# Performance work log

Measured on AMD Instinct MI355X. Metric: run time of the kernel, lower is better.

## Reference

```python
import jax, jax.numpy as jnp
import numpy as np

B, S, D, H = 4, 2048, 1024, 16
DK = D // H


def setup_inputs() -> dict:
    key = jax.random.key(0)
    ks = jax.random.split(key, 12)
    s = 1.0 / np.sqrt(D)
    inp = {
        "q": jax.random.normal(ks[0], (B, S, D), jnp.float32),
        "k": jax.random.normal(ks[1], (B, S, D), jnp.float32),
        "v": jax.random.normal(ks[2], (B, S, D), jnp.float32),
        # causal mask, broadcastable over batch and heads
        "mask": jnp.tril(jnp.ones((S, S), jnp.int32))[None, None, :, :],
        "Wq": jax.random.uniform(ks[3], (D, D), jnp.float32, -s, s),
        "bq": jax.random.uniform(ks[4], (D,), jnp.float32, -s, s),
        "Wk": jax.random.uniform(ks[5], (D, D), jnp.float32, -s, s),
        "bk": jax.random.uniform(ks[6], (D,), jnp.float32, -s, s),
        "Wv": jax.random.uniform(ks[7], (D, D), jnp.float32, -s, s),
        "bv": jax.random.uniform(ks[8], (D,), jnp.float32, -s, s),
        "Wo": jax.random.uniform(ks[9], (D, D), jnp.float32, -s, s),
        "bo": jax.random.uniform(ks[10], (D,), jnp.float32, -s, s),
    }
    return inp


def reference(q, k, v, mask, Wq, bq, Wk, bk, Wv, bv, Wo, bo):
    def split_heads(x):  # [B,S,D] -> [B,H,S,DK]
        return x.reshape(B, S, H, DK).transpose(0, 2, 1, 3)

    qh = split_heads(q @ Wq.T + bq)
    kh = split_heads(k @ Wk.T + bk)
    vh = split_heads(v @ Wv.T + bv)

    scores = jnp.einsum("bhqd,bhkd->bhqk", qh, kh) / jnp.sqrt(jnp.float32(DK))
    scores = jnp.where(mask == 0, jnp.float32(-1e9), scores)
    attn = jax.nn.softmax(scores, axis=-1)
    out = jnp.einsum("bhqk,bhkd->bhqd", attn, vh)
    out = out.transpose(0, 2, 1, 3).reshape(B, S, D)
    return out @ Wo.T + bo
```

## Files before the change

### kernel.cpp

```cpp
#include <hip/hip_runtime.h>
#include <cstdint>

#define Bb 4
#define Ss 2048
#define Dd 1024
#define Hh 16

typedef unsigned short u16;
typedef unsigned int u32;
typedef __attribute__((ext_vector_type(8))) short short8;
typedef __attribute__((ext_vector_type(8))) _Float16 half8;
typedef __attribute__((ext_vector_type(2))) __fp16 fp16x2;
typedef __attribute__((ext_vector_type(4))) float floatx4;
typedef __attribute__((address_space(3))) u32 lds_u32;
typedef const __attribute__((address_space(1))) u32 glob_u32;

__device__ __forceinline__ u16 f2bf(float x) {
  union { float f; u32 u; } v; v.f = x;
  u32 r = v.u + 0x7fffu + ((v.u >> 16) & 1u);
  return (u16)(r >> 16);
}

__global__ __launch_bounds__(256) void cvt_many(const float* __restrict__ s0,
                                                const float* __restrict__ s1,
                                                const float* __restrict__ s2,
                                                const float* __restrict__ s3,
                                                u16* __restrict__ d0,
                                                u16* __restrict__ d1,
                                                u16* __restrict__ d2,
                                                u16* __restrict__ d3, int n8) {
  int z = blockIdx.y;
  const float* s = z == 0 ? s0 : z == 1 ? s1 : z == 2 ? s2 : s3;
  u16* d = z == 0 ? d0 : z == 1 ? d1 : z == 2 ? d2 : d3;
  int i = blockIdx.x * 256 + threadIdx.x;
  if (i >= n8) return;
  const float4* sp = (const float4*)s;
  float4 a = sp[2 * i], b = sp[2 * i + 1];
  u32 w0 = (u32)f2bf(a.x) | ((u32)f2bf(a.y) << 16);
  u32 w1 = (u32)f2bf(a.z) | ((u32)f2bf(a.w) << 16);
  u32 w2 = (u32)f2bf(b.x) | ((u32)f2bf(b.y) << 16);
  u32 w3 = (u32)f2bf(b.z) | ((u32)f2bf(b.w) << 16);
  ((uint4*)d)[i] = make_uint4(w0, w1, w2, w3);
}

template <int MODE>
__device__ __forceinline__ void gemm_body(const u16* __restrict__ A,
                                          const u16* __restrict__ Bw,
                                          const float* __restrict__ bias,
                                          void* __restrict__ Cout, float scale) {
  __shared__ u16 As[128 * 64];
  __shared__ u16 Bs[128 * 64];
  int tid = threadIdx.x;
  int wave = tid >> 6, lane = tid & 63;
  int quad = lane >> 4, l16 = lane & 15;
  int m0 = blockIdx.x * 128, n0 = blockIdx.y * 128;
  int wr = (wave >> 1) * 64, wc = (wave & 1) * 64;
  int s7 = l16 & 7;
  int srow = wave * 8 + (lane >> 3);
  int gcol = (((lane & 7) ^ (lane >> 3)) << 3);

  floatx4 vzero = {0.f, 0.f, 0.f, 0.f};
  floatx4 acc[4][4];
#pragma unroll
  for (int i = 0; i < 4; ++i)
#pragma unroll
    for (int j = 0; j < 4; ++j) acc[i][j] = vzero;

  for (int kt = 0; kt < Dd; kt += 64) {
    __syncthreads();
#pragma unroll
    for (int c = 0; c < 4; ++c) {
      int r = c * 32 + srow;
      __builtin_amdgcn_global_load_lds(
          (glob_u32*)&A[(size_t)(m0 + r) * Dd + kt + gcol],
          (lds_u32*)&As[(c * 32 + wave * 8) * 64], 16, 0, 0);
      __builtin_amdgcn_global_load_lds(
          (glob_u32*)&Bw[(size_t)(n0 + r) * Dd + kt + gcol],
          (lds_u32*)&Bs[(c * 32 + wave * 8) * 64], 16, 0, 0);
    }
    __syncthreads();
#pragma unroll
    for (int kk = 0; kk < 2; ++kk) {
      short8 af[4], bf[4];
#pragma unroll
      for (int i = 0; i < 4; ++i)
        af[i] = *(const short8*)&As[(wr + i * 16 + l16) * 64 + (((quad + 4 * kk) ^ s7) << 3)];
#pragma unroll
      for (int j = 0; j < 4; ++j)
        bf[j] = *(const short8*)&Bs[(wc + j * 16 + l16) * 64 + (((quad + 4 * kk) ^ s7) << 3)];
#pragma unroll
      for (int i = 0; i < 4; ++i)
#pragma unroll
        for (int j = 0; j < 4; ++j)
          acc[i][j] = __builtin_amdgcn_mfma_f32_16x16x32_bf16(af[i], bf[j], acc[i][j], 0, 0, 0);
    }
  }

#pragma unroll
  for (int i = 0; i < 4; ++i) {
#pragma unroll
    for (int j = 0; j < 4; ++j) {
#pragma unroll
      for (int r = 0; r < 4; ++r) {
        int m = m0 + wr + i * 16 + quad * 4 + r;
        int n = n0 + wc + j * 16 + l16;
        float val = (acc[i][j][r] + bias[n]) * scale;
        if (MODE == 0) {
          int b = m >> 11, s = m & (Ss - 1);
          int h = n >> 6, dk = n & 63;
          ((u16*)Cout)[((((size_t)b * Hh + h) * Ss + s) << 6) + dk] = f2bf(val);
        } else {
          ((float*)Cout)[(size_t)m * Dd + n] = val;
        }
      }
    }
  }
}

__global__ __launch_bounds__(256) void gemm_qkv(const u16* qb, const u16* kb, const u16* vb,
                                                const u16* Wq, const u16* Wk, const u16* Wv,
                                                const float* bq, const float* bk, const float* bv,
                                                u16* qo, u16* ko, u16* vo) {
  const float K1 = 0.18033688f;
  int z = blockIdx.z;
  const u16* A = z == 0 ? qb : z == 1 ? kb : vb;
  const u16* W = z == 0 ? Wq : z == 1 ? Wk : Wv;
  const float* bi = z == 0 ? bq : z == 1 ? bk : bv;
  u16* o = z == 0 ? qo : z == 1 ? ko : vo;
  gemm_body<0>(A, W, bi, o, z == 0 ? K1 : 1.0f);
}

__global__ __launch_bounds__(256) void gemm_out(const u16* A, const u16* W,
                                                const float* bi, float* o) {
  gemm_body<1>(A, W, bi, o, 1.0f);
}

__global__ __launch_bounds__(256) void transpose_v(const u16* __restrict__ in,
                                                   _Float16* __restrict__ out) {
  __shared__ u16 T[64 * 72];
  int bh = blockIdx.y, s0 = blockIdx.x * 64, tid = threadIdx.x;
#pragma unroll
  for (int c = 0; c < 2; ++c) {
    int e = c * 2048 + tid * 8;
    int r = e >> 6, col = e & 63;
    *(uint4*)&T[r * 72 + col] = *(const uint4*)&in[((size_t)bh * Ss + s0 + r) * 64 + col];
  }
  __syncthreads();
#pragma unroll
  for (int c = 0; c < 2; ++c) {
    int e = c * 2048 + tid * 8;
    int d = e >> 6, sc = e & 63;
    _Float16 tmp[8];
#pragma unroll
    for (int j = 0; j < 8; ++j) {
      union { u32 u; float f; } cv;
      cv.u = (u32)T[(sc + j) * 72 + d] << 16;
      tmp[j] = (_Float16)cv.f;
    }
    *(uint4*)&out[((size_t)bh * 64 + d) * Ss + s0 + sc] = *(uint4*)tmp;
  }
}

#define MFIX 4.0f
__global__ __launch_bounds__(256) void attn_kernel(const u16* __restrict__ qh,
                                                   const u16* __restrict__ kh,
                                                   const _Float16* __restrict__ vT,
                                                   u16* __restrict__ ctx) {
  __shared__ u16 Kt[64 * 64];
  __shared__ _Float16 Vt[64 * 64];
  __shared__ _Float16 Ps[4][16 * 64];

  int tid = threadIdx.x, w = tid >> 6, lane = tid & 63;
  int quad = lane >> 4, l16 = lane & 15;
  int s7 = l16 & 7, s2 = (l16 & 7) << 1;
  int bh = blockIdx.x;
  int sp = blockIdx.y;
  const u16* Q = qh + (size_t)bh * Ss * 64;
  const u16* K = kh + (size_t)bh * Ss * 64;
  const _Float16* V = vT + (size_t)bh * 64 * Ss;

  int R[2] = {64 * sp + 16 * w, 64 * (31 - sp) + 16 * w};
  short8 qf[2][2];
#pragma unroll
  for (int qm = 0; qm < 2; ++qm)
#pragma unroll
    for (int kk = 0; kk < 2; ++kk)
      qf[qm][kk] = *(const short8*)&Q[(size_t)(R[qm] + l16) * 64 + kk * 32 + quad * 8];

  floatx4 vzero = {0.f, 0.f, 0.f, 0.f};
  floatx4 o[2][4];
#pragma unroll
  for (int qm = 0; qm < 2; ++qm)
#pragma unroll
    for (int nt = 0; nt < 4; ++nt) o[qm][nt] = vzero;
  float l_i[2] = {0.f, 0.f};

  int srow = tid >> 3, kc = tid & 7;
  int nkt = 32 - sp;
  for (int kt = 0; kt < nkt; ++kt) {
    int k0 = kt * 64;
    __syncthreads();
#pragma unroll
    for (int c = 0; c < 2; ++c) {
      int r = c * 32 + srow;
      int wcol = ((kc ^ (r & 7)) << 3);
      *(uint4*)&Kt[r * 64 + wcol] = *(const uint4*)&K[(size_t)(k0 + r) * 64 + kc * 8];
      *(uint4*)&Vt[r * 64 + wcol] = *(const uint4*)&V[(size_t)r * Ss + k0 + kc * 8];
    }
    __syncthreads();

    half8 vf[4][2];
#pragma unroll
    for (int nt = 0; nt < 4; ++nt)
#pragma unroll
      for (int kk = 0; kk < 2; ++kk)
        vf[nt][kk] = *(const half8*)&Vt[(nt * 16 + l16) * 64 + (((quad + 4 * kk) ^ s7) << 3)];

#pragma unroll
    for (int qm = 0; qm < 2; ++qm) {
      int Rq = R[qm];
      if (k0 > Rq + 15) continue;
      floatx4 sc[4];
#pragma unroll
      for (int t4 = 0; t4 < 4; ++t4) {
        short8 kf0 = *(const short8*)&Kt[(t4 * 16 + l16) * 64 + ((quad ^ s7) << 3)];
        short8 kf1 = *(const short8*)&Kt[(t4 * 16 + l16) * 64 + (((quad + 4) ^ s7) << 3)];
        floatx4 s = __builtin_amdgcn_mfma_f32_16x16x32_bf16(kf0, qf[qm][0], vzero, 0, 0, 0);
        sc[t4] = __builtin_amdgcn_mfma_f32_16x16x32_bf16(kf1, qf[qm][1], s, 0, 0, 0);
      }
      int qrow = Rq + l16;
      if (k0 + 63 > Rq) {
#pragma unroll
        for (int t4 = 0; t4 < 4; ++t4)
#pragma unroll
          for (int r = 0; r < 4; ++r) {
            int key = k0 + t4 * 16 + quad * 4 + r;
            if (key > qrow) sc[t4][r] = -3e38f;
          }
      }
      float rs = 0.f;
      _Float16* Pw = &Ps[w][0];
#pragma unroll
      for (int t4 = 0; t4 < 4; ++t4) {
        float p0 = __builtin_amdgcn_exp2f(sc[t4][0] - MFIX);
        float p1 = __builtin_amdgcn_exp2f(sc[t4][1] - MFIX);
        float p2 = __builtin_amdgcn_exp2f(sc[t4][2] - MFIX);
        float p3 = __builtin_amdgcn_exp2f(sc[t4][3] - MFIX);
        rs += (p0 + p1) + (p2 + p3);
        union { fp16x2 h[2]; uint2 u; } cv;
        cv.h[0] = __builtin_amdgcn_cvt_pkrtz(p0, p1);
        cv.h[1] = __builtin_amdgcn_cvt_pkrtz(p2, p3);
        *(uint2*)&Pw[l16 * 64 + (((4 * t4 + quad) ^ s2) << 2)] = cv.u;
      }
      rs += __shfl_xor(rs, 16, 64);
      rs += __shfl_xor(rs, 32, 64);
      l_i[qm] += rs;
#pragma unroll
      for (int kk = 0; kk < 2; ++kk) {
        half8 pf = *(const half8*)&Pw[l16 * 64 + (((8 * kk + 2 * quad) ^ s2) << 2)];
#pragma unroll
        for (int nt = 0; nt < 4; ++nt)
          o[qm][nt] = __builtin_amdgcn_mfma_f32_16x16x32_f16(pf, vf[nt][kk], o[qm][nt], 0, 0, 0);
      }
    }
  }

  int b = bh >> 4, h = bh & 15;
#pragma unroll
  for (int qm = 0; qm < 2; ++qm) {
    float lr[4];
#pragma unroll
    for (int r = 0; r < 4; ++r) lr[r] = __shfl(l_i[qm], quad * 4 + r, 64);
#pragma unroll
    for (int nt = 0; nt < 4; ++nt)
#pragma unroll
      for (int r = 0; r < 4; ++r) {
        int s = R[qm] + quad * 4 + r;
        int dk = nt * 16 + l16;
        ctx[((size_t)b * Ss + s) * Dd + h * 64 + dk] = f2bf(o[qm][nt][r] / lr[r]);
      }
  }
}

extern "C" void kernel_launch(void* const* d_in, const int* in_sizes, int n_in,
                              void* d_out, int out_size, void* d_ws, size_t ws_size,
                              hipStream_t stream) {
  const float* q = (const float*)d_in[0];
  const float* k = (const float*)d_in[1];
  const float* v = (const float*)d_in[2];
  const float* Wq = (const float*)d_in[4];
  const float* bq = (const float*)d_in[5];
  const float* Wk = (const float*)d_in[6];
  const float* bk = (const float*)d_in[7];
  const float* Wv = (const float*)d_in[8];
  const float* bv = (const float*)d_in[9];
  const float* Wo = (const float*)d_in[10];
  const float* bo = (const float*)d_in[11];

  char* ws = (char*)d_ws;
  const size_t MB = 1024 * 1024;
  u16* qb = (u16*)(ws + 0 * MB);
  u16* kb = (u16*)(ws + 16 * MB);
  u16* vb = (u16*)(ws + 32 * MB);
  u16* Wqb = (u16*)(ws + 48 * MB);
  u16* Wkb = (u16*)(ws + 50 * MB);
  u16* Wvb = (u16*)(ws + 52 * MB);
  u16* Wob = (u16*)(ws + 54 * MB);
  u16* qhp = (u16*)(ws + 56 * MB);
  u16* khp = (u16*)(ws + 72 * MB);
  u16* vhp = (u16*)(ws + 88 * MB);
  _Float16* vhT = (_Float16*)kb;
  u16* ctx = qb;

  const int nQKV8 = (Bb * Ss * Dd) / 8;
  const int nW8 = (Dd * Dd) / 8;
  {
    dim3 g(nQKV8 / 256, 3);
    cvt_many<<<g, 256, 0, stream>>>(q, k, v, v, qb, kb, vb, vb, nQKV8);
  }
  {
    dim3 g(nW8 / 256, 4);
    cvt_many<<<g, 256, 0, stream>>>(Wq, Wk, Wv, Wo, Wqb, Wkb, Wvb, Wob, nW8);
  }
  {
    dim3 g((Bb * Ss) / 128, Dd / 128, 3);
    gemm_qkv<<<g, 256, 0, stream>>>(qb, kb, vb, Wqb, Wkb, Wvb, bq, bk, bv, qhp, khp, vhp);
  }
  {
    dim3 g(Ss / 64, Bb * Hh);
    transpose_v<<<g, 256, 0, stream>>>(vhp, vhT);
  }
  {
    dim3 g(Bb * Hh, 16);
    attn_kernel<<<g, 256, 0, stream>>>(qhp, khp, vhT, ctx);
  }
  {
    dim3 g((Bb * Ss) / 128, Dd / 128);
    gemm_out<<<g, 256, 0, stream>>>(ctx, Wob, bo, (float*)d_out);
  }
}
```

Baseline: 339.9 us.

## Double-buffer K/V tiles in LDS with register prefetch and MFMA priority hints

K/V tile staging moves to two LDS buffers. The next tile is prefetched into registers during compute and written to the idle buffer afterwards, so each iteration needs one barrier instead of two. s_setprio is raised around the MFMA sections, and the fixed softmax offset is folded into the QK MFMA accumulator init, which removes a subtraction per score. The cost is double the K/V LDS footprint and more live registers, which may lower occupancy.

```diff
diff --git a/kernel.cpp b/kernel.cpp
--- a/kernel.cpp
+++ b/kernel.cpp
@@ -166,8 +166,8 @@
                                                    const u16* __restrict__ kh,
                                                    const _Float16* __restrict__ vT,
                                                    u16* __restrict__ ctx) {
-  __shared__ u16 Kt[64 * 64];
-  __shared__ _Float16 Vt[64 * 64];
+  __shared__ u16 Kt[2][64 * 64];
+  __shared__ _Float16 Vt[2][64 * 64];
   __shared__ _Float16 Ps[4][16 * 64];
 
   int tid = threadIdx.x, w = tid >> 6, lane = tid & 63;
@@ -188,6 +188,7 @@
       qf[qm][kk] = *(const short8*)&Q[(size_t)(R[qm] + l16) * 64 + kk * 32 + quad * 8];
 
   floatx4 vzero = {0.f, 0.f, 0.f, 0.f};
+  floatx4 minit = {-MFIX, -MFIX, -MFIX, -MFIX};
   floatx4 o[2][4];
 #pragma unroll
   for (int qm = 0; qm < 2; ++qm)
@@ -196,38 +197,57 @@
   float l_i[2] = {0.f, 0.f};
 
   int srow = tid >> 3, kc = tid & 7;
+  int r1s = srow + 32;
+  int wcol = ((kc ^ (srow & 7)) << 3);
   int nkt = 32 - sp;
+
+  uint4 kr0, kr1, vr0, vr1;
+#define LOADT(KT)                                                          \
+  {                                                                        \
+    int _k0 = (KT) * 64;                                                   \
+    kr0 = *(const uint4*)&K[(size_t)(_k0 + srow) * 64 + kc * 8];           \
+    kr1 = *(const uint4*)&K[(size_t)(_k0 + r1s) * 64 + kc * 8];            \
+    vr0 = *(const uint4*)&V[(size_t)srow * Ss + _k0 + kc * 8];             \
+    vr1 = *(const uint4*)&V[(size_t)r1s * Ss + _k0 + kc * 8];              \
+  }
+#define WRITET(P)                                                          \
+  {                                                                        \
+    *(uint4*)&Kt[P][srow * 64 + wcol] = kr0;                               \
+    *(uint4*)&Kt[P][r1s * 64 + wcol] = kr1;                                \
+    *(uint4*)&Vt[P][srow * 64 + wcol] = vr0;                               \
+    *(uint4*)&Vt[P][r1s * 64 + wcol] = vr1;                                \
+  }
+
+  LOADT(0);
+  WRITET(0);
+  LOADT(1);
+
+  int p = 0;
   for (int kt = 0; kt < nkt; ++kt) {
     int k0 = kt * 64;
     __syncthreads();
-#pragma unroll
-    for (int c = 0; c < 2; ++c) {
-      int r = c * 32 + srow;
-      int wcol = ((kc ^ (r & 7)) << 3);
-      *(uint4*)&Kt[r * 64 + wcol] = *(const uint4*)&K[(size_t)(k0 + r) * 64 + kc * 8];
-      *(uint4*)&Vt[r * 64 + wcol] = *(const uint4*)&V[(size_t)r * Ss + k0 + kc * 8];
-    }
-    __syncthreads();
 
     half8 vf[4][2];
 #pragma unroll
     for (int nt = 0; nt < 4; ++nt)
 #pragma unroll
       for (int kk = 0; kk < 2; ++kk)
-        vf[nt][kk] = *(const half8*)&Vt[(nt * 16 + l16) * 64 + (((quad + 4 * kk) ^ s7) << 3)];
+        vf[nt][kk] = *(const half8*)&Vt[p][(nt * 16 + l16) * 64 + (((quad + 4 * kk) ^ s7) << 3)];
 
 #pragma unroll
     for (int qm = 0; qm < 2; ++qm) {
       int Rq = R[qm];
       if (k0 > Rq + 15) continue;
       floatx4 sc[4];
+      __builtin_amdgcn_s_setprio(1);
 #pragma unroll
       for (int t4 = 0; t4 < 4; ++t4) {
-        short8 kf0 = *(const short8*)&Kt[(t4 * 16 + l16) * 64 + ((quad ^ s7) << 3)];
-        short8 kf1 = *(const short8*)&Kt[(t4 * 16 + l16) * 64 + (((quad + 4) ^ s7) << 3)];
-        floatx4 s = __builtin_amdgcn_mfma_f32_16x16x32_bf16(kf0, qf[qm][0], vzero, 0, 0, 0);
+        short8 kf0 = *(const short8*)&Kt[p][(t4 * 16 + l16) * 64 + ((quad ^ s7) << 3)];
+        short8 kf1 = *(const short8*)&Kt[p][(t4 * 16 + l16) * 64 + (((quad + 4) ^ s7) << 3)];
+        floatx4 s = __builtin_amdgcn_mfma_f32_16x16x32_bf16(kf0, qf[qm][0], minit, 0, 0, 0);
         sc[t4] = __builtin_amdgcn_mfma_f32_16x16x32_bf16(kf1, qf[qm][1], s, 0, 0, 0);
       }
+      __builtin_amdgcn_s_setprio(0);
       int qrow = Rq + l16;
       if (k0 + 63 > Rq) {
 #pragma unroll
@@ -242,10 +262,10 @@
       _Float16* Pw = &Ps[w][0];
 #pragma unroll
       for (int t4 = 0; t4 < 4; ++t4) {
-        float p0 = __builtin_amdgcn_exp2f(sc[t4][0] - MFIX);
-        float p1 = __builtin_amdgcn_exp2f(sc[t4][1] - MFIX);
-        float p2 = __builtin_amdgcn_exp2f(sc[t4][2] - MFIX);
-        float p3 = __builtin_amdgcn_exp2f(sc[t4][3] - MFIX);
+        float p0 = __builtin_amdgcn_exp2f(sc[t4][0]);
+        float p1 = __builtin_amdgcn_exp2f(sc[t4][1]);
+        float p2 = __builtin_amdgcn_exp2f(sc[t4][2]);
+        float p3 = __builtin_amdgcn_exp2f(sc[t4][3]);
         rs += (p0 + p1) + (p2 + p3);
         union { fp16x2 h[2]; uint2 u; } cv;
         cv.h[0] = __builtin_amdgcn_cvt_pkrtz(p0, p1);
@@ -255,6 +275,7 @@
       rs += __shfl_xor(rs, 16, 64);
       rs += __shfl_xor(rs, 32, 64);
       l_i[qm] += rs;
+      __builtin_amdgcn_s_setprio(1);
 #pragma unroll
       for (int kk = 0; kk < 2; ++kk) {
         half8 pf = *(const half8*)&Pw[l16 * 64 + (((8 * kk + 2 * quad) ^ s2) << 2)];
@@ -262,8 +283,17 @@
         for (int nt = 0; nt < 4; ++nt)
           o[qm][nt] = __builtin_amdgcn_mfma_f32_16x16x32_f16(pf, vf[nt][kk], o[qm][nt], 0, 0, 0);
       }
-    }
-  }
+      __builtin_amdgcn_s_setprio(0);
+    }
+
+    if (kt + 1 < nkt) {
+      WRITET(p ^ 1);
+      if (kt + 2 < nkt) LOADT(kt + 2);
+    }
+    p ^= 1;
+  }
+#undef LOADT
+#undef WRITET
 
   int b = bh >> 4, h = bh & 15;
 #pragma unroll
```

Measured after the change: 331.2 us. -2.6%, faster.

## Rewrite attention inner loop with 32x32 MFMA, async LDS double buffering, register P

Applied to the files above, without the earlier changes.

Rewrites the attention kernel so each wave handles 32 query rows with 32x32x16 MFMA tiles. K/V tiles are double-buffered in LDS via global_load_lds, so the next tile's load overlaps compute and one barrier per tile is dropped. The P matrix is reshuffled in registers with v_permlane32_swap instead of a round trip through LDS. Causal masking skips the upper half of diagonal tiles, and setprio hints are added around the MFMA sections. This cuts LDS traffic and sync overhead at the cost of higher register pressure and more complex lane mapping.

```diff
diff --git a/kernel.cpp b/kernel.cpp
--- a/kernel.cpp
+++ b/kernel.cpp
@@ -12,6 +12,7 @@
 typedef __attribute__((ext_vector_type(8))) _Float16 half8;
 typedef __attribute__((ext_vector_type(2))) __fp16 fp16x2;
 typedef __attribute__((ext_vector_type(4))) float floatx4;
+typedef __attribute__((ext_vector_type(16))) float floatx16;
 typedef __attribute__((address_space(3))) u32 lds_u32;
 typedef const __attribute__((address_space(1))) u32 glob_u32;
 
@@ -19,6 +20,18 @@
   union { float f; u32 u; } v; v.f = x;
   u32 r = v.u + 0x7fffu + ((v.u >> 16) & 1u);
   return (u16)(r >> 16);
+}
+
+__device__ __forceinline__ u32 pk2(float a, float b) {
+  union { fp16x2 h; u32 u; } cv;
+  cv.h = __builtin_amdgcn_cvt_pkrtz(a, b);
+  return cv.u;
+}
+
+__device__ __forceinline__ half8 h8_from(u32 a, u32 b, u32 c, u32 d) {
+  union { u32 u[4]; half8 h; } t;
+  t.u[0] = a; t.u[1] = b; t.u[2] = c; t.u[3] = d;
+  return t.h;
 }
 
 __global__ __launch_bounds__(256) void cvt_many(const float* __restrict__ s0,
@@ -162,123 +175,154 @@
 }
 
 #define MFIX 4.0f
+#define SW(a, b) asm("v_permlane32_swap_b32 %0, %1" : "+v"(a), "+v"(b))
+#define VRD(CH, NT) \
+  (*(const half8*)&Vt[p][((NT) * 32 + l31) * 64 + ((((CH) + hi) ^ s7b) << 3)])
+
+#define TILE_BODY(NST, MASKED)                                                \
+  do {                                                                        \
+    short8 kf0[4], kf1[4];                                                    \
+    _Pragma("unroll") for (int m = 0; m < 4; ++m) {                           \
+      kf0[m] = *(const short8*)&Kt[p][l31 * 64 + (((2 * m + hi) ^ s7b) << 3)];\
+      if (NST == 2)                                                           \
+        kf1[m] = *(const short8*)&Kt[p][(32 + l31) * 64 +                     \
+                                        (((2 * m + hi) ^ s7b) << 3)];         \
+    }                                                                         \
+    floatx16 sc0, sc1;                                                        \
+    _Pragma("unroll") for (int r = 0; r < 16; ++r) {                          \
+      sc0[r] = -MFIX;                                                         \
+      sc1[r] = -MFIX;                                                         \
+    }                                                                         \
+    __builtin_amdgcn_s_setprio(1);                                            \
+    _Pragma("unroll") for (int m = 0; m < 4; ++m) {                           \
+      sc0 = __builtin_amdgcn_mfma_f32_32x32x16_bf16(kf0[m], qf[m], sc0, 0, 0, 0); \
+      if (NST == 2)                                                           \
+        sc1 = __builtin_amdgcn_mfma_f32_32x32x16_bf16(kf1[m], qf[m], sc1, 0, 0, 0); \
+    }                                                                         \
+    __builtin_amdgcn_s_setprio(0);                                            \
+    if (MASKED) {                                                             \
+      int qrow = Rq + l31;                                                    \
+      _Pragma("unroll") for (int r = 0; r < 16; ++r) {                        \
+        int key = k0 + 4 * hi + (r & 3) + 8 * (r >> 2);                       \
+        if (key > qrow) sc0[r] = -3e38f;                                      \
+        if (NST == 2 && key + 32 > qrow) sc1[r] = -3e38f;                     \
+      }                                                                       \
+    }                                                                         \
+    u32 c0[8], c1[8];                                                         \
+    float rs = 0.f;                                                           \
+    _Pragma("unroll") for (int j = 0; j < 8; ++j) {                           \
+      float p0 = __builtin_amdgcn_exp2f(sc0[2 * j]);                          \
+      float p1 = __builtin_amdgcn_exp2f(sc0[2 * j + 1]);                      \
+      rs += p0 + p1;                                                          \
+      c0[j] = pk2(p0, p1);                                                    \
+      if (NST == 2) {                                                         \
+        float p2 = __builtin_amdgcn_exp2f(sc1[2 * j]);                        \
+        float p3 = __builtin_amdgcn_exp2f(sc1[2 * j + 1]);                    \
+        rs += p2 + p3;                                                        \
+        c1[j] = pk2(p2, p3);                                                  \
+      }                                                                       \
+    }                                                                         \
+    l_part += rs;                                                             \
+    SW(c0[0], c0[2]); SW(c0[1], c0[3]); SW(c0[4], c0[6]); SW(c0[5], c0[7]);   \
+    if (NST == 2) {                                                           \
+      SW(c1[0], c1[2]); SW(c1[1], c1[3]); SW(c1[4], c1[6]); SW(c1[5], c1[7]); \
+    }                                                                         \
+    __builtin_amdgcn_s_setprio(1);                                            \
+    {                                                                         \
+      half8 pa = h8_from(c0[0], c0[1], c0[2], c0[3]);                         \
+      o0 = __builtin_amdgcn_mfma_f32_32x32x16_f16(pa, VRD(0, 0), o0, 0, 0, 0);\
+      o1 = __builtin_amdgcn_mfma_f32_32x32x16_f16(pa, VRD(0, 1), o1, 0, 0, 0);\
+      half8 pb = h8_from(c0[4], c0[5], c0[6], c0[7]);                         \
+      o0 = __builtin_amdgcn_mfma_f32_32x32x16_f16(pb, VRD(2, 0), o0, 0, 0, 0);\
+      o1 = __builtin_amdgcn_mfma_f32_32x32x16_f16(pb, VRD(2, 1), o1, 0, 0, 0);\
+      if (NST == 2) {                                                         \
+        half8 pc = h8_from(c1[0], c1[1], c1[2], c1[3]);                       \
+        o0 = __builtin_amdgcn_mfma_f32_32x32x16_f16(pc, VRD(4, 0), o0, 0, 0, 0); \
+        o1 = __builtin_amdgcn_mfma_f32_32x32x16_f16(pc, VRD(4, 1), o1, 0, 0, 0); \
+        half8 pd = h8_from(c1[4], c1[5], c1[6], c1[7]);                       \
+        o0 = __builtin_amdgcn_mfma_f32_32x32x16_f16(pd, VRD(6, 0), o0, 0, 0, 0); \
+        o1 = __builtin_amdgcn_mfma_f32_32x32x16_f16(pd, VRD(6, 1), o1, 0, 0, 0); \
+      }                                                                       \
+    }                                                                         \
+    __builtin_amdgcn_s_setprio(0);                                            \
+  } while (0)
+
 __global__ __launch_bounds__(256) void attn_kernel(const u16* __restrict__ qh,
                                                    const u16* __restrict__ kh,
                                                    const _Float16* __restrict__ vT,
                                                    u16* __restrict__ ctx) {
-  __shared__ u16 Kt[64 * 64];
-  __shared__ _Float16 Vt[64 * 64];
-  __shared__ _Float16 Ps[4][16 * 64];
+  __shared__ u16 Kt[2][64 * 64];
+  __shared__ _Float16 Vt[2][64 * 64];
 
   int tid = threadIdx.x, w = tid >> 6, lane = tid & 63;
-  int quad = lane >> 4, l16 = lane & 15;
-  int s7 = l16 & 7, s2 = (l16 & 7) << 1;
+  int hi = lane >> 5, l31 = lane & 31, s7b = lane & 7;
   int bh = blockIdx.x;
   int sp = blockIdx.y;
   const u16* Q = qh + (size_t)bh * Ss * 64;
   const u16* K = kh + (size_t)bh * Ss * 64;
   const _Float16* V = vT + (size_t)bh * 64 * Ss;
 
-  int R[2] = {64 * sp + 16 * w, 64 * (31 - sp) + 16 * w};
-  short8 qf[2][2];
-#pragma unroll
-  for (int qm = 0; qm < 2; ++qm)
-#pragma unroll
-    for (int kk = 0; kk < 2; ++kk)
-      qf[qm][kk] = *(const short8*)&Q[(size_t)(R[qm] + l16) * 64 + kk * 32 + quad * 8];
-
-  floatx4 vzero = {0.f, 0.f, 0.f, 0.f};
-  floatx4 o[2][4];
-#pragma unroll
-  for (int qm = 0; qm < 2; ++qm)
-#pragma unroll
-    for (int nt = 0; nt < 4; ++nt) o[qm][nt] = vzero;
-  float l_i[2] = {0.f, 0.f};
-
-  int srow = tid >> 3, kc = tid & 7;
+  int Rq = (w < 2) ? 64 * sp + 32 * w : 64 * (31 - sp) + 32 * (w - 2);
+
+  short8 qf[4];
+#pragma unroll
+  for (int m = 0; m < 4; ++m)
+    qf[m] = *(const short8*)&Q[(size_t)(Rq + l31) * 64 + m * 16 + hi * 8];
+
+  floatx16 o0, o1;
+#pragma unroll
+  for (int r = 0; r < 16; ++r) { o0[r] = 0.f; o1[r] = 0.f; }
+  float l_part = 0.f;
+
+  int lrow = w * 8 + (lane >> 3);
+  int g8 = ((lane & 7) ^ (lane >> 3)) << 3;
   int nkt = 32 - sp;
+
+#define STAGE(P, KT)                                                          \
+  do {                                                                        \
+    int _k0 = (KT) * 64;                                                      \
+    __builtin_amdgcn_global_load_lds(                                         \
+        (glob_u32*)&K[(size_t)(_k0 + lrow) * 64 + g8],                        \
+        (lds_u32*)&Kt[P][w * 512], 16, 0, 0);                                 \
+    __builtin_amdgcn_global_load_lds(                                         \
+        (glob_u32*)&K[(size_t)(_k0 + 32 + lrow) * 64 + g8],                   \
+        (lds_u32*)&Kt[P][2048 + w * 512], 16, 0, 0);                          \
+    __builtin_amdgcn_global_load_lds(                                         \
+        (glob_u32*)&V[(size_t)lrow * Ss + _k0 + g8],                          \
+        (lds_u32*)&Vt[P][w * 512], 16, 0, 0);                                 \
+    __builtin_amdgcn_global_load_lds(                                         \
+        (glob_u32*)&V[(size_t)(32 + lrow) * Ss + _k0 + g8],                   \
+        (lds_u32*)&Vt[P][2048 + w * 512], 16, 0, 0);                          \
+  } while (0)
+
+  STAGE(0, 0);
+
+  int p = 0;
   for (int kt = 0; kt < nkt; ++kt) {
     int k0 = kt * 64;
     __syncthreads();
-#pragma unroll
-    for (int c = 0; c < 2; ++c) {
-      int r = c * 32 + srow;
-      int wcol = ((kc ^ (r & 7)) << 3);
-      *(uint4*)&Kt[r * 64 + wcol] = *(const uint4*)&K[(size_t)(k0 + r) * 64 + kc * 8];
-      *(uint4*)&Vt[r * 64 + wcol] = *(const uint4*)&V[(size_t)r * Ss + k0 + kc * 8];
-    }
-    __syncthreads();
-
-    half8 vf[4][2];
-#pragma unroll
-    for (int nt = 0; nt < 4; ++nt)
-#pragma unroll
-      for (int kk = 0; kk < 2; ++kk)
-        vf[nt][kk] = *(const half8*)&Vt[(nt * 16 + l16) * 64 + (((quad + 4 * kk) ^ s7) << 3)];
-
-#pragma unroll
-    for (int qm = 0; qm < 2; ++qm) {
-      int Rq = R[qm];
-      if (k0 > Rq + 15) continue;
-      floatx4 sc[4];
-#pragma unroll
-      for (int t4 = 0; t4 < 4; ++t4) {
-        short8 kf0 = *(const short8*)&Kt[(t4 * 16 + l16) * 64 + ((quad ^ s7) << 3)];
-        short8 kf1 = *(const short8*)&Kt[(t4 * 16 + l16) * 64 + (((quad + 4) ^ s7) << 3)];
-        floatx4 s = __builtin_amdgcn_mfma_f32_16x16x32_bf16(kf0, qf[qm][0], vzero, 0, 0, 0);
-        sc[t4] = __builtin_amdgcn_mfma_f32_16x16x32_bf16(kf1, qf[qm][1], s, 0, 0, 0);
-      }
-      int qrow = Rq + l16;
-      if (k0 + 63 > Rq) {
-#pragma unroll
-        for (int t4 = 0; t4 < 4; ++t4)
-#pragma unroll
-          for (int r = 0; r < 4; ++r) {
-            int key = k0 + t4 * 16 + quad * 4 + r;
-            if (key > qrow) sc[t4][r] = -3e38f;
-          }
-      }
-      float rs = 0.f;
-      _Float16* Pw = &Ps[w][0];
-#pragma unroll
-      for (int t4 = 0; t4 < 4; ++t4) {
-        float p0 = __builtin_amdgcn_exp2f(sc[t4][0] - MFIX);
-        float p1 = __builtin_amdgcn_exp2f(sc[t4][1] - MFIX);
-        float p2 = __builtin_amdgcn_exp2f(sc[t4][2] - MFIX);
-        float p3 = __builtin_amdgcn_exp2f(sc[t4][3] - MFIX);
-        rs += (p0 + p1) + (p2 + p3);
-        union { fp16x2 h[2]; uint2 u; } cv;
-        cv.h[0] = __builtin_amdgcn_cvt_pkrtz(p0, p1);
-        cv.h[1] = __builtin_amdgcn_cvt_pkrtz(p2, p3);
-        *(uint2*)&Pw[l16 * 64 + (((4 * t4 + quad) ^ s2) << 2)] = cv.u;
-      }
-      rs += __shfl_xor(rs, 16, 64);
-      rs += __shfl_xor(rs, 32, 64);
-      l_i[qm] += rs;
-#pragma unroll
-      for (int kk = 0; kk < 2; ++kk) {
-        half8 pf = *(const half8*)&Pw[l16 * 64 + (((8 * kk + 2 * quad) ^ s2) << 2)];
-#pragma unroll
-        for (int nt = 0; nt < 4; ++nt)
-          o[qm][nt] = __builtin_amdgcn_mfma_f32_16x16x32_f16(pf, vf[nt][kk], o[qm][nt], 0, 0, 0);
-      }
-    }
-  }
-
+    if (kt + 1 < nkt) STAGE(p ^ 1, kt + 1);
+
+    if (k0 + 63 <= Rq) {
+      TILE_BODY(2, false);
+    } else if (k0 <= Rq + 31) {
+      if (k0 + 32 <= Rq + 31) TILE_BODY(2, true);
+      else TILE_BODY(1, true);
+    }
+    p ^= 1;
+  }
+#undef STAGE
+
+  float l2 = l_part + __shfl_xor(l_part, 32, 64);
+  float linv = 1.0f / l2;
   int b = bh >> 4, h = bh & 15;
 #pragma unroll
-  for (int qm = 0; qm < 2; ++qm) {
-    float lr[4];
-#pragma unroll
-    for (int r = 0; r < 4; ++r) lr[r] = __shfl(l_i[qm], quad * 4 + r, 64);
-#pragma unroll
-    for (int nt = 0; nt < 4; ++nt)
-#pragma unroll
-      for (int r = 0; r < 4; ++r) {
-        int s = R[qm] + quad * 4 + r;
-        int dk = nt * 16 + l16;
-        ctx[((size_t)b * Ss + s) * Dd + h * 64 + dk] = f2bf(o[qm][nt][r] / lr[r]);
-      }
+  for (int r = 0; r < 16; ++r) {
+    int qi = (r & 3) + 8 * (r >> 2) + 4 * hi;
+    float li = __shfl(linv, qi, 64);
+    size_t base = ((size_t)b * Ss + Rq + qi) * Dd + h * 64 + l31;
+    ctx[base] = f2bf(o0[r] * li);
+    ctx[base + 32] = f2bf(o1[r] * li);
   }
 }
 
```

Measured after the change: 335.3 us. Within noise of the previous version (-1.3%).
